# Optimization experiments

Measured on AMD Instinct MI355X. Metric: run time of the kernel, lower is better.

The kernel has to match this reference:

```python
import jax, jax.numpy as jnp
import numpy as np

B, T, C = 4, 1024, 1024
L, H = 4, 8
D = C // H          # head_size = 128
F = 4 * C           # ff_hd = 4096
EPS = 1e-5          # torch LayerNorm default


def _ln(x, s, b):
    m = jnp.mean(x, axis=-1, keepdims=True)
    v = jnp.var(x, axis=-1, keepdims=True)
    return (x - m) * jax.lax.rsqrt(v + EPS) * s + b


def setup_inputs() -> dict:
    key = jax.random.key(0)
    ks = jax.random.split(key, 16)
    std = 0.02
    return {
        "x": jax.random.normal(ks[0], (B, T, C), jnp.float32),
        "pos_emb": jax.random.normal(ks[1], (T, C), jnp.float32) * std,
        # per-head QKV projections, stacked over layers: [L, H, C, D]
        "Wq": jax.random.normal(ks[2], (L, H, C, D), jnp.float32) * std,
        "Wk": jax.random.normal(ks[3], (L, H, C, D), jnp.float32) * std,
        "Wv": jax.random.normal(ks[4], (L, H, C, D), jnp.float32) * std,
        "Wo": jax.random.normal(ks[5], (L, C, C), jnp.float32) * std,
        "bo": jnp.zeros((L, C), jnp.float32),
        "ln1_s": jnp.ones((L, C), jnp.float32),
        "ln1_b": jnp.zeros((L, C), jnp.float32),
        "ln2_s": jnp.ones((L, C), jnp.float32),
        "ln2_b": jnp.zeros((L, C), jnp.float32),
        "W1": jax.random.normal(ks[6], (L, C, F), jnp.float32) * std,
        "b1": jnp.zeros((L, F), jnp.float32),
        "W2": jax.random.normal(ks[7], (L, F, C), jnp.float32) * std,
        "b2": jnp.zeros((L, C), jnp.float32),
        "lnf_s": jnp.ones((C,), jnp.float32),
        "lnf_b": jnp.zeros((C,), jnp.float32),
    }


def _encoder(x, pos_emb, Wq, Wk, Wv, Wo, bo, ln1_s, ln1_b, ln2_s, ln2_b,
             W1, b1, W2, b2, lnf_s, lnf_b):
    x = x + pos_emb  # [B,T,C]
    scale = D ** -0.5

    def step(h_x, p):
        (wq, wk, wv, wo, bo_, l1s, l1b, l2s, l2b, w1, b1_, w2, b2_) = p
        xn = _ln(h_x, l1s, l1b)
        q = jnp.einsum('btc,hcd->bhtd', xn, wq)
        k = jnp.einsum('btc,hcd->bhtd', xn, wk)
        v = jnp.einsum('btc,hcd->bhtd', xn, wv)
        att = jax.nn.softmax(jnp.einsum('bhtd,bhsd->bhts', q, k) * scale, axis=-1)
        o = jnp.einsum('bhts,bhsd->bhtd', att, v)          # [B,H,T,D]
        o = o.transpose(0, 2, 1, 3).reshape(B, T, C)        # concat heads
        h_x = h_x + o @ wo + bo_
        xn2 = _ln(h_x, l2s, l2b)
        h_x = h_x + jax.nn.relu(xn2 @ w1 + b1_) @ w2 + b2_
        # att returned as [H,B,T,T] to mirror per-head list ordering
        return h_x, att.transpose(1, 0, 2, 3)

    x, atts = jax.lax.scan(step, x, (Wq, Wk, Wv, Wo, bo, ln1_s, ln1_b,
                                     ln2_s, ln2_b, W1, b1, W2, b2))
    x = _ln(x, lnf_s, lnf_b)
    return x, atts  # atts: [L, H, B, T, T]


def reference(x, pos_emb, Wq, Wk, Wv, Wo, bo, ln1_s, ln1_b, ln2_s, ln2_b,
              W1, b1, W2, b2, lnf_s, lnf_b):
    return _encoder(x, pos_emb, Wq, Wk, Wv, Wo, bo, ln1_s, ln1_b, ln2_s, ln2_b,
                    W1, b1, W2, b2, lnf_s, lnf_b)
```

## Files before the change

### kernel.cpp

```cpp
#include <hip/hip_runtime.h>
#include <hip/hip_bf16.h>

typedef __attribute__((ext_vector_type(8))) short bf16x8;
typedef __attribute__((ext_vector_type(4))) float f32x4;
typedef __hip_bfloat16 bf16;

__global__ __launch_bounds__(256) void transpose_cvt(
    const float* __restrict__ in, bf16* __restrict__ out, int R, int Cc)
{
  __shared__ float tile[32][33];
  long base = (long)blockIdx.z * R * Cc;
  int c0 = blockIdx.x * 32, r0 = blockIdx.y * 32;
  int tx = threadIdx.x & 31, ty = threadIdx.x >> 5;
  #pragma unroll
  for (int i = 0; i < 32; i += 8)
    tile[ty + i][tx] = in[base + (long)(r0 + ty + i) * Cc + (c0 + tx)];
  __syncthreads();
  #pragma unroll
  for (int i = 0; i < 32; i += 8)
    out[base + (long)(c0 + ty + i) * R + (r0 + tx)] =
        __float2bfloat16(tile[tx][ty + i]);
}

__global__ __launch_bounds__(256) void add_pos(
    const float* __restrict__ x, const float* __restrict__ pos,
    float* __restrict__ h)
{
  int i = blockIdx.x * 1024 + threadIdx.x;
  #pragma unroll
  for (int j = 0; j < 4; ++j) {
    int idx = i + j * 256;
    h[idx] = x[idx] + pos[idx & ((1 << 20) - 1)];
  }
}

__device__ inline float wave_sum(float v) {
  #pragma unroll
  for (int o = 32; o; o >>= 1) v += __shfl_down(v, o, 64);
  return v;
}

template<bool F32OUT>
__global__ __launch_bounds__(256) void layernorm_k(
    const float* __restrict__ x, const float* __restrict__ s,
    const float* __restrict__ b, void* __restrict__ outv)
{
  __shared__ float red[8];
  long row = blockIdx.x;
  const float* xr = x + (row << 10);
  int t = threadIdx.x;
  float v[4]; float sum = 0.f, sq = 0.f;
  #pragma unroll
  for (int i = 0; i < 4; ++i) {
    v[i] = xr[t + i * 256];
    sum += v[i]; sq += v[i] * v[i];
  }
  sum = wave_sum(sum); sq = wave_sum(sq);
  if ((t & 63) == 0) { red[t >> 6] = sum; red[4 + (t >> 6)] = sq; }
  __syncthreads();
  sum = red[0] + red[1] + red[2] + red[3];
  sq  = red[4] + red[5] + red[6] + red[7];
  float mean = sum * (1.f / 1024.f);
  float var  = sq * (1.f / 1024.f) - mean * mean;
  float rstd = rsqrtf(var + 1e-5f);
  #pragma unroll
  for (int i = 0; i < 4; ++i) {
    int c = t + i * 256;
    float y = (v[i] - mean) * rstd * s[c] + b[c];
    if (F32OUT) ((float*)outv)[(row << 10) + c] = y;
    else        ((bf16*)outv)[(row << 10) + c] = __float2bfloat16(y);
  }
}

__global__ __launch_bounds__(512, 2) void fused_attn(
    const bf16* __restrict__ q, const bf16* __restrict__ kb,
    const bf16* __restrict__ vT, float* __restrict__ attL,
    bf16* __restrict__ o)
{
  __shared__ __align__(16) bf16 p_lds[64 * 1032];
  __shared__ float red[2][8][64];
  const int tid  = threadIdx.x;
  const int wave = tid >> 6, lane = tid & 63;
  const int quad = lane >> 4, l16 = lane & 15;
  const int bm = blockIdx.x, bz = blockIdx.y;
  const int b = bz >> 3, hh = bz & 7;
  const bf16* qb  = q  + ((long)bz << 17) + ((long)bm << 13);
  const bf16* kbz = kb + ((long)bz << 17);
  const bf16* vbz = vT + ((long)bz << 17);
  const int wn = wave << 7;

  f32x4 acc[4][8] = {};
  #pragma unroll
  for (int kk = 0; kk < 4; ++kk) {
    bf16x8 af[4];
    #pragma unroll
    for (int i = 0; i < 4; ++i)
      af[i] = *(const bf16x8*)(qb + (i * 16 + l16) * 128 + kk * 32 + quad * 8);
    #pragma unroll
    for (int jg = 0; jg < 8; jg += 4) {
      bf16x8 bfr[4];
      #pragma unroll
      for (int j = 0; j < 4; ++j)
        bfr[j] = *(const bf16x8*)(kbz +
            (long)(wn + (jg + j) * 16 + l16) * 128 + kk * 32 + quad * 8);
      #pragma unroll
      for (int j = 0; j < 4; ++j)
        #pragma unroll
        for (int i = 0; i < 4; ++i)
          acc[i][jg + j] = __builtin_amdgcn_mfma_f32_16x16x32_bf16(
              af[i], bfr[j], acc[i][jg + j], 0, 0, 0);
    }
  }

  float mx[4][4];
  #pragma unroll
  for (int i = 0; i < 4; ++i)
    #pragma unroll
    for (int r = 0; r < 4; ++r) {
      float m = -3.4e38f;
      #pragma unroll
      for (int j = 0; j < 8; ++j) m = fmaxf(m, acc[i][j][r]);
      #pragma unroll
      for (int off = 1; off < 16; off <<= 1) m = fmaxf(m, __shfl_xor(m, off, 64));
      mx[i][r] = m;
    }
  if (l16 == 0) {
    #pragma unroll
    for (int i = 0; i < 4; ++i)
      #pragma unroll
      for (int r = 0; r < 4; ++r)
        red[0][wave][i * 16 + quad * 4 + r] = mx[i][r];
  }
  __syncthreads();
  #pragma unroll
  for (int i = 0; i < 4; ++i)
    #pragma unroll
    for (int r = 0; r < 4; ++r) {
      int row = i * 16 + quad * 4 + r;
      float m = red[0][0][row];
      #pragma unroll
      for (int w = 1; w < 8; ++w) m = fmaxf(m, red[0][w][row]);
      mx[i][r] = m;
    }

  const float scale = 0.08838834764831845f;
  float inv[4][4];
  #pragma unroll
  for (int i = 0; i < 4; ++i)
    #pragma unroll
    for (int r = 0; r < 4; ++r) {
      float s = 0.f;
      #pragma unroll
      for (int j = 0; j < 8; ++j) {
        float e = __expf((acc[i][j][r] - mx[i][r]) * scale);
        acc[i][j][r] = e; s += e;
      }
      #pragma unroll
      for (int off = 1; off < 16; off <<= 1) s += __shfl_xor(s, off, 64);
      inv[i][r] = s;
    }
  if (l16 == 0) {
    #pragma unroll
    for (int i = 0; i < 4; ++i)
      #pragma unroll
      for (int r = 0; r < 4; ++r)
        red[1][wave][i * 16 + quad * 4 + r] = inv[i][r];
  }
  __syncthreads();
  #pragma unroll
  for (int i = 0; i < 4; ++i)
    #pragma unroll
    for (int r = 0; r < 4; ++r) {
      int row = i * 16 + quad * 4 + r;
      float s = 0.f;
      #pragma unroll
      for (int w = 0; w < 8; ++w) s += red[1][w][row];
      inv[i][r] = 1.f / s;
    }

  long ob = ((long)(hh * 4 + b) << 20) + ((long)(bm * 64) << 10);
  #pragma unroll
  for (int i = 0; i < 4; ++i)
    #pragma unroll
    for (int r = 0; r < 4; ++r) {
      int row = i * 16 + quad * 4 + r;
      float iv = inv[i][r];
      #pragma unroll
      for (int j = 0; j < 8; ++j) {
        float p = acc[i][j][r] * iv;
        int col = wn + j * 16 + l16;
        attL[ob + ((long)row << 10) + col] = p;
        p_lds[row * 1032 + col] = __float2bfloat16(p);
      }
    }
  __syncthreads();

  const int wm2 = (wave >> 2) << 5;
  const int wd  = (wave & 3) << 5;
  f32x4 acc2[2][2] = {};
  #pragma unroll 4
  for (int s0 = 0; s0 < 1024; s0 += 32) {
    bf16x8 pa[2], vv[2];
    #pragma unroll
    for (int i = 0; i < 2; ++i)
      pa[i] = *(const bf16x8*)(p_lds + (wm2 + i * 16 + l16) * 1032 + s0 + quad * 8);
    #pragma unroll
    for (int j = 0; j < 2; ++j)
      vv[j] = *(const bf16x8*)(vbz + (long)(wd + j * 16 + l16) * 1024 + s0 + quad * 8);
    #pragma unroll
    for (int i = 0; i < 2; ++i)
      #pragma unroll
      for (int j = 0; j < 2; ++j)
        acc2[i][j] = __builtin_amdgcn_mfma_f32_16x16x32_bf16(
            pa[i], vv[j], acc2[i][j], 0, 0, 0);
  }
  long ob2 = ((long)b << 20) + ((long)bm << 16) + (hh << 7);
  #pragma unroll
  for (int i = 0; i < 2; ++i)
    #pragma unroll
    for (int j = 0; j < 2; ++j)
      #pragma unroll
      for (int r = 0; r < 4; ++r) {
        int t = wm2 + i * 16 + quad * 4 + r;
        int d = wd + j * 16 + l16;
        o[ob2 + ((long)t << 10) + d] = __float2bfloat16(acc2[i][j][r]);
      }
}

enum { EPI_BHTD = 0, EPI_VT, EPI_SCORES, EPI_ATTV, EPI_RES, EPI_RELU };

template<int EPI>
__global__ __launch_bounds__(256, 2) void gemm_bt(
    const bf16* __restrict__ A, const bf16* __restrict__ Bt,
    void* __restrict__ Cout, const float* __restrict__ bias, float scale,
    int M, int N, int K, int lda, int ldb, long sAb, long sBb)
{
  __shared__ __align__(16) bf16 sA[128 * 64];
  __shared__ __align__(16) bf16 sB[128 * 64];
  const int tid = threadIdx.x;
  const int bn = blockIdx.x, bm = blockIdx.y, bz = blockIdx.z;
  const bf16* Ab = A + bz * sAb + (long)bm * 128 * lda;
  const bf16* Bb = Bt + bz * sBb + (long)bn * 128 * ldb;
  const int wave = tid >> 6, lane = tid & 63;
  const int wm = (wave >> 1) * 64, wn = (wave & 1) * 64;
  const int quad = lane >> 4, l16 = lane & 15;

  f32x4 acc[4][4] = {};

  for (int k0 = 0; k0 < K; k0 += 64) {
    #pragma unroll
    for (int i = 0; i < 4; ++i) {
      int c = i * 256 + tid;
      int row = c >> 3, col = (c & 7) << 3;
      int ldsoff = (i * 256 + (tid & ~63)) << 3;
      __builtin_amdgcn_global_load_lds(
          (const __attribute__((address_space(1))) void*)(Ab + (long)row * lda + (k0 + col)),
          (__attribute__((address_space(3))) void*)(sA + ldsoff), 16, 0, 0);
      __builtin_amdgcn_global_load_lds(
          (const __attribute__((address_space(1))) void*)(Bb + (long)row * ldb + (k0 + col)),
          (__attribute__((address_space(3))) void*)(sB + ldsoff), 16, 0, 0);
    }
    __syncthreads();
    #pragma unroll
    for (int kk = 0; kk < 64; kk += 32) {
      bf16x8 af[4], bfr[4];
      #pragma unroll
      for (int i = 0; i < 4; ++i) {
        af[i]  = *(const bf16x8*)(sA + (wm + i * 16 + l16) * 64 + kk + quad * 8);
        bfr[i] = *(const bf16x8*)(sB + (wn + i * 16 + l16) * 64 + kk + quad * 8);
      }
      #pragma unroll
      for (int i = 0; i < 4; ++i)
        #pragma unroll
        for (int j = 0; j < 4; ++j)
          acc[i][j] = __builtin_amdgcn_mfma_f32_16x16x32_bf16(
              af[i], bfr[j], acc[i][j], 0, 0, 0);
    }
    __syncthreads();
  }

  #pragma unroll
  for (int i = 0; i < 4; ++i) {
    #pragma unroll
    for (int j = 0; j < 4; ++j) {
      #pragma unroll
      for (int r = 0; r < 4; ++r) {
        int m = (bm << 7) + wm + i * 16 + (quad << 2) + r;
        int n = (bn << 7) + wn + j * 16 + l16;
        float v = acc[i][j][r];
        if (EPI == EPI_BHTD) {
          long idx = ((long)((m >> 10) * 8 + (n >> 7)) << 17) +
                     ((long)(m & 1023) << 7) + (n & 127);
          ((bf16*)Cout)[idx] = __float2bfloat16(v);
        } else if (EPI == EPI_VT) {
          long idx = ((long)((m >> 10) * 8 + (n >> 7)) << 17) +
                     ((long)(n & 127) << 10) + (m & 1023);
          ((bf16*)Cout)[idx] = __float2bfloat16(v);
        } else if (EPI == EPI_SCORES) {
          long idx = ((long)((bz & 7) * 4 + (bz >> 3)) << 20) +
                     ((long)m << 10) + n;
          ((float*)Cout)[idx] = v * scale;
        } else if (EPI == EPI_ATTV) {
          long idx = ((long)(bz >> 3) << 20) + ((long)m << 10) +
                     ((bz & 7) << 7) + n;
          ((bf16*)Cout)[idx] = __float2bfloat16(v);
        } else if (EPI == EPI_RES) {
          long idx = (long)m * N + n;
          ((float*)Cout)[idx] += v + bias[n];
        } else {
          long idx = (long)m * N + n;
          ((bf16*)Cout)[idx] = __float2bfloat16(fmaxf(v + bias[n], 0.f));
        }
      }
    }
  }
}

extern "C" void kernel_launch(void* const* d_in, const int* in_sizes, int n_in,
                              void* d_out, int out_size, void* d_ws, size_t ws_size,
                              hipStream_t stream)
{
  const float* x     = (const float*)d_in[0];
  const float* pos   = (const float*)d_in[1];
  const float* Wq    = (const float*)d_in[2];
  const float* Wk    = (const float*)d_in[3];
  const float* Wv    = (const float*)d_in[4];
  const float* Wo    = (const float*)d_in[5];
  const float* bo    = (const float*)d_in[6];
  const float* ln1_s = (const float*)d_in[7];
  const float* ln1_b = (const float*)d_in[8];
  const float* ln2_s = (const float*)d_in[9];
  const float* ln2_b = (const float*)d_in[10];
  const float* W1    = (const float*)d_in[11];
  const float* b1    = (const float*)d_in[12];
  const float* W2    = (const float*)d_in[13];
  const float* b2    = (const float*)d_in[14];
  const float* lnf_s = (const float*)d_in[15];
  const float* lnf_b = (const float*)d_in[16];
  float* out = (float*)d_out;

  char* w = (char*)d_ws;
  float* h  = (float*)w;
  bf16* xn  = (bf16*)(w + (16l  << 20));
  bf16* q   = (bf16*)(w + (24l  << 20));
  bf16* kb  = (bf16*)(w + (32l  << 20));
  bf16* vT  = (bf16*)(w + (40l  << 20));
  bf16* o   = (bf16*)(w + (48l  << 20));
  bf16* big = (bf16*)(w + (56l  << 20));
  bf16* WqT = (bf16*)(w + (120l << 20));
  bf16* WkT = (bf16*)(w + (128l << 20));
  bf16* WvT = (bf16*)(w + (136l << 20));
  bf16* WoT = (bf16*)(w + (144l << 20));
  bf16* W1T = (bf16*)(w + (152l << 20));
  bf16* W2T = (bf16*)(w + (184l << 20));

  dim3 blk(256);
  transpose_cvt<<<dim3(4, 32, 32),  blk, 0, stream>>>(Wq, WqT, 1024, 128);
  transpose_cvt<<<dim3(4, 32, 32),  blk, 0, stream>>>(Wk, WkT, 1024, 128);
  transpose_cvt<<<dim3(4, 32, 32),  blk, 0, stream>>>(Wv, WvT, 1024, 128);
  transpose_cvt<<<dim3(32, 32, 4),  blk, 0, stream>>>(Wo, WoT, 1024, 1024);
  transpose_cvt<<<dim3(128, 32, 4), blk, 0, stream>>>(W1, W1T, 1024, 4096);
  transpose_cvt<<<dim3(32, 128, 4), blk, 0, stream>>>(W2, W2T, 4096, 1024);

  add_pos<<<4096, blk, 0, stream>>>(x, pos, h);

  for (int l = 0; l < 4; ++l) {
    layernorm_k<false><<<4096, blk, 0, stream>>>(h, ln1_s + l * 1024, ln1_b + l * 1024, xn);
    gemm_bt<EPI_BHTD><<<dim3(8, 32, 1), blk, 0, stream>>>(
        xn, WqT + (long)l * 1048576, q, nullptr, 0.f, 4096, 1024, 1024, 1024, 1024, 0, 0);
    gemm_bt<EPI_BHTD><<<dim3(8, 32, 1), blk, 0, stream>>>(
        xn, WkT + (long)l * 1048576, kb, nullptr, 0.f, 4096, 1024, 1024, 1024, 1024, 0, 0);
    gemm_bt<EPI_VT><<<dim3(8, 32, 1), blk, 0, stream>>>(
        xn, WvT + (long)l * 1048576, vT, nullptr, 0.f, 4096, 1024, 1024, 1024, 1024, 0, 0);

    float* attL = out + 4194304l + (long)l * 33554432l;
    fused_attn<<<dim3(16, 32), dim3(512), 0, stream>>>(q, kb, vT, attL, o);

    gemm_bt<EPI_RES><<<dim3(8, 32, 1), blk, 0, stream>>>(
        o, WoT + (long)l * 1048576, h, bo + l * 1024, 0.f, 4096, 1024, 1024, 1024, 1024, 0, 0);

    layernorm_k<false><<<4096, blk, 0, stream>>>(h, ln2_s + l * 1024, ln2_b + l * 1024, xn);
    gemm_bt<EPI_RELU><<<dim3(32, 32, 1), blk, 0, stream>>>(
        xn, W1T + (long)l * 4194304, big, b1 + l * 4096, 0.f, 4096, 4096, 1024, 1024, 1024, 0, 0);
    gemm_bt<EPI_RES><<<dim3(8, 32, 1), blk, 0, stream>>>(
        big, W2T + (long)l * 4194304, h, b2 + l * 1024, 0.f, 4096, 1024, 4096, 4096, 4096, 0, 0);
  }
  layernorm_k<true><<<4096, blk, 0, stream>>>(h, lnf_s, lnf_b, out);
}
```

Baseline: 2.262 ms.

## Merge QKV projections into one launch and split-K residual GEMMs with atomics

The three Q/K/V projection GEMMs become a single launch whose z index selects the weight slice and the output layout (BHTD or transposed V). The output-projection and second FFN GEMMs are split along K into two halves that accumulate into the residual with atomicAdd, with the bias added only by the first half. The aim is to double the block count on the 256-block GEMMs so the GPU is better filled and to cut launch count. In exchange it adds float atomic traffic, makes the accumulation order nondeterministic, and depends on the q/k/vT buffers sitting at fixed strides.

```diff
diff --git a/kernel.cpp b/kernel.cpp
--- a/kernel.cpp
+++ b/kernel.cpp
@@ -227,7 +227,7 @@
       }
 }
 
-enum { EPI_BHTD = 0, EPI_VT, EPI_SCORES, EPI_ATTV, EPI_RES, EPI_RELU };
+enum { EPI_BHTD = 0, EPI_VT, EPI_QKV, EPI_RES, EPI_RES_AT, EPI_RELU };
 
 template<int EPI>
 __global__ __launch_bounds__(256, 2) void gemm_bt(
@@ -296,17 +296,22 @@
           long idx = ((long)((m >> 10) * 8 + (n >> 7)) << 17) +
                      ((long)(n & 127) << 10) + (m & 1023);
           ((bf16*)Cout)[idx] = __float2bfloat16(v);
-        } else if (EPI == EPI_SCORES) {
-          long idx = ((long)((bz & 7) * 4 + (bz >> 3)) << 20) +
-                     ((long)m << 10) + n;
-          ((float*)Cout)[idx] = v * scale;
-        } else if (EPI == EPI_ATTV) {
-          long idx = ((long)(bz >> 3) << 20) + ((long)m << 10) +
-                     ((bz & 7) << 7) + n;
-          ((bf16*)Cout)[idx] = __float2bfloat16(v);
+        } else if (EPI == EPI_QKV) {
+          bf16* dst = (bf16*)Cout + (long)bz * 4194304;
+          long idx;
+          if (bz < 2)
+            idx = ((long)((m >> 10) * 8 + (n >> 7)) << 17) +
+                  ((long)(m & 1023) << 7) + (n & 127);
+          else
+            idx = ((long)((m >> 10) * 8 + (n >> 7)) << 17) +
+                  ((long)(n & 127) << 10) + (m & 1023);
+          dst[idx] = __float2bfloat16(v);
         } else if (EPI == EPI_RES) {
           long idx = (long)m * N + n;
           ((float*)Cout)[idx] += v + bias[n];
+        } else if (EPI == EPI_RES_AT) {
+          long idx = (long)m * N + n;
+          atomicAdd(&((float*)Cout)[idx], v + (bz == 0 ? bias[n] : 0.f));
         } else {
           long idx = (long)m * N + n;
           ((bf16*)Cout)[idx] = __float2bfloat16(fmaxf(v + bias[n], 0.f));
@@ -366,24 +371,24 @@
 
   for (int l = 0; l < 4; ++l) {
     layernorm_k<false><<<4096, blk, 0, stream>>>(h, ln1_s + l * 1024, ln1_b + l * 1024, xn);
-    gemm_bt<EPI_BHTD><<<dim3(8, 32, 1), blk, 0, stream>>>(
-        xn, WqT + (long)l * 1048576, q, nullptr, 0.f, 4096, 1024, 1024, 1024, 1024, 0, 0);
-    gemm_bt<EPI_BHTD><<<dim3(8, 32, 1), blk, 0, stream>>>(
-        xn, WkT + (long)l * 1048576, kb, nullptr, 0.f, 4096, 1024, 1024, 1024, 1024, 0, 0);
-    gemm_bt<EPI_VT><<<dim3(8, 32, 1), blk, 0, stream>>>(
-        xn, WvT + (long)l * 1048576, vT, nullptr, 0.f, 4096, 1024, 1024, 1024, 1024, 0, 0);
+    gemm_bt<EPI_QKV><<<dim3(8, 32, 3), blk, 0, stream>>>(
+        xn, WqT + (long)l * 1048576, q, nullptr, 0.f,
+        4096, 1024, 1024, 1024, 1024, 0, 4194304l);
 
     float* attL = out + 4194304l + (long)l * 33554432l;
     fused_attn<<<dim3(16, 32), dim3(512), 0, stream>>>(q, kb, vT, attL, o);
 
-    gemm_bt<EPI_RES><<<dim3(8, 32, 1), blk, 0, stream>>>(
-        o, WoT + (long)l * 1048576, h, bo + l * 1024, 0.f, 4096, 1024, 1024, 1024, 1024, 0, 0);
+    gemm_bt<EPI_RES_AT><<<dim3(8, 32, 2), blk, 0, stream>>>(
+        o, WoT + (long)l * 1048576, h, bo + l * 1024, 0.f,
+        4096, 1024, 512, 1024, 1024, 512, 512);
 
     layernorm_k<false><<<4096, blk, 0, stream>>>(h, ln2_s + l * 1024, ln2_b + l * 1024, xn);
     gemm_bt<EPI_RELU><<<dim3(32, 32, 1), blk, 0, stream>>>(
-        xn, W1T + (long)l * 4194304, big, b1 + l * 4096, 0.f, 4096, 4096, 1024, 1024, 1024, 0, 0);
-    gemm_bt<EPI_RES><<<dim3(8, 32, 1), blk, 0, stream>>>(
-        big, W2T + (long)l * 4194304, h, b2 + l * 1024, 0.f, 4096, 1024, 4096, 4096, 4096, 0, 0);
+        xn, W1T + (long)l * 4194304, big, b1 + l * 4096, 0.f,
+        4096, 4096, 1024, 1024, 1024, 0, 0);
+    gemm_bt<EPI_RES_AT><<<dim3(8, 32, 2), blk, 0, stream>>>(
+        big, W2T + (long)l * 4194304, h, b2 + l * 1024, 0.f,
+        4096, 1024, 2048, 4096, 4096, 2048, 2048);
   }
   layernorm_k<true><<<4096, blk, 0, stream>>>(h, lnf_s, lnf_b, out);
 }
```

Result: faster. 1.970 ms (-12.9%).
